# Performance work log

Measured on AMD Instinct MI355X. Metric: run time of the kernel, lower is better.

## Reference

```python
import jax, jax.numpy as jnp
import numpy as np

EPS = 1e-5  # PNA std-aggregator epsilon
N_NODES, N_EDGES, F_DIM, N_LAYERS = 50000, 800000, 64, 3


def setup_inputs() -> dict:
    key = jax.random.key(0)
    ks = jax.random.split(key, 6)
    x = jax.random.normal(ks[0], (N_NODES, F_DIM), jnp.float32)
    edge_index = jax.random.randint(ks[1], (2, N_EDGES), 0, N_NODES, jnp.int32)
    # Per-layer parameters, stacked on a leading layer axis.
    pre_w = jax.random.normal(ks[2], (N_LAYERS, 2 * F_DIM, F_DIM), jnp.float32) / np.sqrt(2 * F_DIM).astype(np.float32)
    pre_b = jnp.zeros((N_LAYERS, F_DIM), jnp.float32)
    post_w = jax.random.normal(ks[3], (N_LAYERS, 13 * F_DIM, F_DIM), jnp.float32) / np.sqrt(13 * F_DIM).astype(np.float32)
    post_b = jnp.zeros((N_LAYERS, F_DIM), jnp.float32)
    lin_w = jax.random.normal(ks[4], (N_LAYERS, F_DIM, F_DIM), jnp.float32) / np.sqrt(F_DIM).astype(np.float32)
    lin_b = jnpp = jnp.zeros((N_LAYERS, F_DIM), jnp.float32)
    return dict(x=x, edge_index=edge_index, pre_w=pre_w, pre_b=pre_b,
                post_w=post_w, post_b=post_b, lin_w=lin_w, lin_b=lin_b)


def reference(x, edge_index, pre_w, pre_b, post_w, post_b, lin_w, lin_b):
    src, dst = edge_index[0], edge_index[1]
    n = x.shape[0]
    # In-degree of aggregation targets (clamped to >=1, as in PyG DegreeScalerAggregation).
    deg = jax.ops.segment_sum(jnp.ones_like(dst, dtype=x.dtype), dst, num_segments=n)
    has_edge = (deg > 0)[:, None]
    deg_c = jnp.maximum(deg, 1.0)[:, None]              # [N,1]
    log_deg = jnp.log(deg_c + 1.0)                      # [N,1]
    avg_log = jnp.mean(log_deg)
    amp = log_deg / avg_log                              # amplification scaler
    att = avg_log / log_deg                              # attenuation scaler

    h = x
    for l in range(pre_w.shape[0]):
        # message: pre_nn(cat([x_i, x_j]))  -> [E, F]
        m = jnp.concatenate([h[dst], h[src]], axis=-1) @ pre_w[l] + pre_b[l]
        # fused multi-aggregator scatter-reduce per target node
        s1 = jax.ops.segment_sum(m, dst, num_segments=n)
        s2 = jax.ops.segment_sum(m * m, dst, num_segments=n)
        mean = s1 / deg_c
        std = jnp.sqrt(jax.nn.relu(s2 / deg_c - mean * mean) + EPS)
        mx = jnp.where(has_edge, jax.ops.segment_max(m, dst, num_segments=n), 0.0)
        mn = jnp.where(has_edge, jax.ops.segment_min(m, dst, num_segments=n), 0.0)
        agg = jnp.concatenate([mean, mx, mn, std], axis=-1)        # [N, 4F]
        scaled = jnp.concatenate([agg, agg * amp, agg * att], -1)  # [N, 12F]
        # post_nn(cat([x, scaled])) then final lin, plus residual shortcut
        out = jnp.concatenate([h, scaled], axis=-1) @ post_w[l] + post_b[l]
        out = out @ lin_w[l] + lin_b[l]
        h = out + h
    return h
```

## Files before the change

kernel.cpp:

```cpp
#include <hip/hip_runtime.h>
#include <math.h>

#define EPSV 1e-5f
#define EPB3 4096
#define NBP 256
#define CAP 6144
#define CAPS (CAP + 768)

typedef short s16x8 __attribute__((ext_vector_type(8)));
typedef float f32x4 __attribute__((ext_vector_type(4)));
typedef unsigned short u16;
typedef unsigned short u16x4 __attribute__((ext_vector_type(4)));

#define MFMA(a, b, c) __builtin_amdgcn_mfma_f32_16x16x32_bf16(a, b, c, 0, 0, 0)

__device__ inline u16 f2bf(float f) {
    unsigned u = __float_as_uint(f);
    return (u16)((u + 0x7FFF + ((u >> 16) & 1)) >> 16);
}
__device__ inline float bf2f(u16 h) { return __uint_as_float(((unsigned)h) << 16); }

__device__ inline void split8(const float4& a, const float4& b, s16x8& hv, s16x8& lv) {
    float f[8] = {a.x, a.y, a.z, a.w, b.x, b.y, b.z, b.w};
#pragma unroll
    for (int i = 0; i < 8; ++i) {
        u16 h = f2bf(f[i]);
        hv[i] = (short)h;
        lv[i] = (short)f2bf(f[i] - bf2f(h));
    }
}

__global__ __launch_bounds__(512) void k_pre1(
    const int* __restrict__ src, const int* __restrict__ dst, int E,
    int* __restrict__ bucketCursor, unsigned* __restrict__ edgeTmp,
    const float* __restrict__ pre_w, const float* __restrict__ post_w,
    const float* __restrict__ post_b, const float* __restrict__ lin_w,
    const float* __restrict__ lin_b, u16* __restrict__ WpT_hi,
    u16* __restrict__ WpT_lo, u16* __restrict__ WT_hi, u16* __restrict__ WT_lo,
    float* __restrict__ bpp, int NB1) {
    __shared__ int cnt[NBP], loff[NBP], lpos[NBP], gbase[NBP], sbuf[NBP];
    __shared__ unsigned stage[EPB3];
    int t = threadIdx.x;
    if ((int)blockIdx.x < NB1) {
        int base = blockIdx.x * EPB3;
        int cntE = min(EPB3, E - base);
        if (t < NBP) cnt[t] = 0;
        __syncthreads();
        unsigned ed[8];
#pragma unroll
        for (int j = 0; j < 8; ++j) {
            int idx = j * 512 + t;
            if (idx < cntE) {
                int e = base + idx;
                unsigned s = (unsigned)src[e];
                unsigned d = (unsigned)dst[e];
                ed[j] = ((d >> 8) << 24) | ((d & 255u) << 16) | s;
                atomicAdd(&cnt[d >> 8], 1);
            } else ed[j] = 0xFFFFFFFFu;
        }
        __syncthreads();
        if (t < NBP) sbuf[t] = cnt[t];
        __syncthreads();
        for (int o = 1; o < NBP; o <<= 1) {
            int v = 0;
            if (t < NBP && t >= o) v = sbuf[t - o];
            __syncthreads();
            if (t < NBP) sbuf[t] += v;
            __syncthreads();
        }
        if (t < NBP) {
            loff[t] = sbuf[t] - cnt[t];
            lpos[t] = sbuf[t] - cnt[t];
            gbase[t] = (cnt[t] > 0) ? atomicAdd(&bucketCursor[t], cnt[t]) : 0;
        }
        __syncthreads();
#pragma unroll
        for (int j = 0; j < 8; ++j) {
            if (ed[j] != 0xFFFFFFFFu) {
                int b = ed[j] >> 24;
                int p = atomicAdd(&lpos[b], 1);
                stage[p] = ed[j];
            }
        }
        __syncthreads();
        for (int i = t; i < cntE; i += 512) {
            unsigned pr = stage[i];
            int b = pr >> 24;
            int pos = gbase[b] + (i - loff[b]);
            if (pos < CAP) edgeTmp[(size_t)b * CAP + pos] = pr;
        }
        return;
    }
    int wq = blockIdx.x - NB1;
    int l = wq / 449;
    int bx = wq - l * 449;
    if (bx < 320) {
        if (t < 192) {
            int k = bx, j = t;
            int third = j >> 6, c = j & 63;
            float out = 0.f;
            int r = -1;
            if (k < 64) r = (third == 0) ? k : -1;
            else        r = 64 + third * 256 + (k - 64);
            if (r >= 0) {
                const float* pw = post_w + (size_t)(l * 832 + r) * 64;
                const float* lw = lin_w + (size_t)l * 64 * 64;
                float s = 0.f;
                for (int kk = 0; kk < 64; ++kk) s += pw[kk] * lw[kk * 64 + c];
                out = s;
            }
            u16 h = f2bf(out);
            size_t o = ((size_t)l * 192 + j) * 320 + k;
            WT_hi[o] = h;
            WT_lo[o] = f2bf(out - bf2f(h));
        }
    } else if (bx < 448) {
        if (t < 64) {
            int c = bx - 320, k = t;
            float v = pre_w[(size_t)l * 8192 + (size_t)(k + (c >= 64 ? 64 : 0)) * 64 + (c & 63)];
            u16 h = f2bf(v);
            size_t o = ((size_t)l * 128 + c) * 64 + k;
            WpT_hi[o] = h;
            WpT_lo[o] = f2bf(v - bf2f(h));
        }
    } else {
        if (t < 64) {
            int c = t;
            const float* pb = post_b + l * 64;
            const float* lw = lin_w + (size_t)l * 64 * 64;
            float s = lin_b[l * 64 + c];
            for (int k = 0; k < 64; ++k) s += pb[k] * lw[k * 64 + c];
            bpp[l * 64 + c] = s;
        }
    }
}

__global__ __launch_bounds__(512) void k_pre2(
    const unsigned* __restrict__ edgeTmp, const int* __restrict__ bucketCur,
    int* __restrict__ deg, int* __restrict__ offs, float* __restrict__ lsum,
    u16* __restrict__ srcSorted,
    const float* __restrict__ x, const u16* __restrict__ WpT_hi,
    const u16* __restrict__ WpT_lo, const float* __restrict__ pre_b,
    u16* __restrict__ Ph, u16* __restrict__ Qh,
    int N, int E, int NB) {
    __shared__ __align__(16) char smem[55296];
    int t = threadIdx.x;
    if ((int)blockIdx.x < NB) {
        int* scnt = (int*)smem;
        int* sbuf = (int*)(smem + 1024);
        int* lcur = (int*)(smem + 2048);
        int* lofs = (int*)(smem + 3072);
        float* fred = (float*)(smem + 4096);
        u16* stageSrc = (u16*)(smem + 5120);
        int* cntPs = (int*)(smem + 5120 + CAPS * 2);
        int b = blockIdx.x;
        int n0 = b << 8;
        int nodes = min(256, N - n0);
        if (t < NBP) { lcur[t] = 0; scnt[t] = 0; }
        __syncthreads();
        int cnt = min(bucketCur[b], CAP);
        const unsigned* ebase = edgeTmp + (size_t)b * CAP;
        for (int i = t; i < cnt; i += 512) atomicAdd(&lcur[(ebase[i] >> 16) & 255], 1);
        __syncthreads();
        float ls = 0.f;
        int d = 0, dP = 0;
        if (t < nodes) {
            d = lcur[t];
            deg[n0 + t] = d;
            ls = logf(fmaxf((float)d, 1.f) + 1.f);
            dP = (d + 3) & ~3;
        }
        if (t < 256) fred[t] = ls;
        if (t < NBP) sbuf[t] = dP;
        __syncthreads();
        for (int o = 1; o < NBP; o <<= 1) {
            int v = 0;
            if (t < NBP && t >= o) v = sbuf[t - o];
            __syncthreads();
            if (t < NBP) sbuf[t] += v;
            __syncthreads();
        }
        if (t < NBP) lofs[t] = sbuf[t] - dP;
        if (t < nodes) offs[n0 + t] = b * CAPS + (sbuf[t] - dP);
        if (t == NBP - 1) *cntPs = sbuf[t];
        __syncthreads();
        for (int o = 128; o > 0; o >>= 1) {
            if (t < o) fred[t] += fred[t + o];
            __syncthreads();
        }
        if (t == 0) atomicAdd(lsum, fred[0]);
        for (int i = t; i < cnt; i += 512) {
            unsigned p = ebase[i];
            int dl = (p >> 16) & 255;
            int r = atomicAdd(&scnt[dl], 1);
            stageSrc[lofs[dl] + r] = (u16)(p & 0xFFFFu);
        }
        __syncthreads();
        if (t < nodes && (d & 3)) {
            int lp = lofs[t];
            u16 lastv = stageSrc[lp + d - 1];
            for (int k = d; k < dP; ++k) stageSrc[lp + k] = lastv;
        }
        __syncthreads();
        int cntP = *cntPs;
        for (int i = t; i < cntP; i += 512) srcSorted[(size_t)b * CAPS + i] = stageSrc[i];
        return;
    }
    u16* Ah = (u16*)smem;
    u16* Al = (u16*)(smem + 9216);
    u16* Bh = (u16*)(smem + 18432);
    u16* Bl = (u16*)(smem + 36864);
    int rows0 = ((int)blockIdx.x - NB) * 64;
    int wid = t >> 6, lane = t & 63;
    int quad = lane >> 4, l16 = lane & 15;
    int wm = wid & 1, wn = wid >> 1;
    if (t < 256) {
#pragma unroll
        for (int it = 0; it < 2; ++it) {
            int task = it * 256 + t;
            int r = task >> 3, seg = task & 7;
            int row = rows0 + r;
            float4 v0 = make_float4(0.f, 0.f, 0.f, 0.f), v1 = v0;
            if (row < N) {
                v0 = *(const float4*)&x[(size_t)row * 64 + seg * 8];
                v1 = *(const float4*)&x[(size_t)row * 64 + seg * 8 + 4];
            }
            s16x8 hv, lv;
            split8(v0, v1, hv, lv);
            *(s16x8*)&Ah[r * 72 + seg * 8] = hv;
            *(s16x8*)&Al[r * 72 + seg * 8] = lv;
        }
#pragma unroll
        for (int it = 0; it < 4; ++it) {
            int task = it * 256 + t;
            int c = task >> 3, seg = task & 7;
            *(s16x8*)&Bh[c * 72 + seg * 8] = *(const s16x8*)&WpT_hi[(size_t)c * 64 + seg * 8];
            *(s16x8*)&Bl[c * 72 + seg * 8] = *(const s16x8*)&WpT_lo[(size_t)c * 64 + seg * 8];
        }
    }
    __syncthreads();
    if (t < 256) {
        f32x4 acc[2][4];
#pragma unroll
        for (int mt = 0; mt < 2; ++mt)
#pragma unroll
            for (int tt = 0; tt < 4; ++tt) acc[mt][tt] = (f32x4){0.f, 0.f, 0.f, 0.f};
#pragma unroll
        for (int c = 0; c < 2; ++c) {
            s16x8 ah[2], al[2];
#pragma unroll
            for (int mt = 0; mt < 2; ++mt) {
                int r = wm * 32 + mt * 16 + l16;
                ah[mt] = *(s16x8*)&Ah[r * 72 + c * 32 + quad * 8];
                al[mt] = *(s16x8*)&Al[r * 72 + c * 32 + quad * 8];
            }
#pragma unroll
            for (int tt = 0; tt < 4; ++tt) {
                int cc = wn * 64 + tt * 16 + l16;
                s16x8 bh = *(s16x8*)&Bh[cc * 72 + c * 32 + quad * 8];
                s16x8 bl = *(s16x8*)&Bl[cc * 72 + c * 32 + quad * 8];
#pragma unroll
                for (int mt = 0; mt < 2; ++mt) {
                    acc[mt][tt] = MFMA(ah[mt], bh, acc[mt][tt]);
                    acc[mt][tt] = MFMA(ah[mt], bl, acc[mt][tt]);
                    if (wn == 0) acc[mt][tt] = MFMA(al[mt], bh, acc[mt][tt]);
                }
            }
        }
#pragma unroll
        for (int mt = 0; mt < 2; ++mt)
#pragma unroll
            for (int tt = 0; tt < 4; ++tt) {
                int col = wn * 64 + tt * 16 + l16;
#pragma unroll
                for (int r = 0; r < 4; ++r) {
                    int row = rows0 + wm * 32 + mt * 16 + quad * 4 + r;
                    if (row >= N) continue;
                    float v = acc[mt][tt][r];
                    if (col < 64) Ph[(size_t)row * 64 + col] = f2bf(v + pre_b[col]);
                    else          Qh[(size_t)row * 64 + (col - 64)] = f2bf(v);
                }
            }
    }
}


__global__ __launch_bounds__(256) void k_agg(const u16* __restrict__ Ph,
                                             const u16* __restrict__ Qh,
                                             const int* __restrict__ offs,
                                             const int* __restrict__ degp,
                                             const u16* __restrict__ ss,
                                             u16* __restrict__ AGGh, int N) {
    int w = threadIdx.x >> 6, lane = threadIdx.x & 63;
    int g = lane >> 4;
    int f4b = (lane & 15) << 3;
    int node = blockIdx.x * 16 + w * 4 + g;
    int nc = min(node, N - 1);
    int beg = offs[nc];
    int d = (node < N) ? degp[nc] : 0;
    int dP = (d + 3) & ~3;
    int end = beg + dP;
    int mdP = dP;
    mdP = max(mdP, __shfl_xor(mdP, 16));
    mdP = max(mdP, __shfl_xor(mdP, 32));
    int trips = mdP >> 2;

    float sum0 = 0.f, sum1 = 0.f, sum2 = 0.f, sum3 = 0.f;
    float sq0 = 0.f, sq1 = 0.f, sq2 = 0.f, sq3 = 0.f;
    float mx0 = -3.4e38f, mx1 = -3.4e38f, mx2 = -3.4e38f, mx3 = -3.4e38f;
    float mn0 = 3.4e38f, mn1 = 3.4e38f, mn2 = 3.4e38f, mn3 = 3.4e38f;

    const char* qbase = (const char*)Qh;

#define ACC4(LO, HI)                                                        \
    {                                                                       \
        float q0 = __uint_as_float((LO) << 16);                             \
        float q1 = __uint_as_float((LO) & 0xFFFF0000u);                     \
        float q2 = __uint_as_float((HI) << 16);                             \
        float q3 = __uint_as_float((HI) & 0xFFFF0000u);                     \
        sum0 += q0; sq0 = fmaf(q0, q0, sq0);                                \
        mx0 = fmaxf(mx0, q0); mn0 = fminf(mn0, q0);                         \
        sum1 += q1; sq1 = fmaf(q1, q1, sq1);                                \
        mx1 = fmaxf(mx1, q1); mn1 = fminf(mn1, q1);                         \
        sum2 += q2; sq2 = fmaf(q2, q2, sq2);                                \
        mx2 = fmaxf(mx2, q2); mn2 = fminf(mn2, q2);                         \
        sum3 += q3; sq3 = fmaf(q3, q3, sq3);                                \
        mx3 = fmaxf(mx3, q3); mn3 = fminf(mn3, q3);                         \
    }

    int e = beg;
    for (int it = 0; it < trips; ++it, e += 4) {
        if (e < end) {
            uint2 sw = *(const uint2*)(ss + e);
            unsigned a0 = ((sw.x & 0xFFFFu) << 7) | (unsigned)f4b;
            unsigned a1 = ((sw.x >> 16) << 7) | (unsigned)f4b;
            unsigned a2 = ((sw.y & 0xFFFFu) << 7) | (unsigned)f4b;
            unsigned a3 = ((sw.y >> 16) << 7) | (unsigned)f4b;
            uint2 qa = *(const uint2*)(qbase + a0);
            uint2 qb = *(const uint2*)(qbase + a1);
            uint2 qc = *(const uint2*)(qbase + a2);
            uint2 qd = *(const uint2*)(qbase + a3);
            ACC4(qa.x, qa.y);
            ACC4(qb.x, qb.y);
            ACC4(qc.x, qc.y);
            ACC4(qd.x, qd.y);
        }
    }
#undef ACC4

    if (d & 3) {
        unsigned sl = ss[beg + d - 1];
        uint2 ql = *(const uint2*)(qbase + ((sl << 7) | (unsigned)f4b));
        float padf = (float)(dP - d);
        float qL0 = __uint_as_float(ql.x << 16);
        float qL1 = __uint_as_float(ql.x & 0xFFFF0000u);
        float qL2 = __uint_as_float(ql.y << 16);
        float qL3 = __uint_as_float(ql.y & 0xFFFF0000u);
        float t0 = padf * qL0, t1 = padf * qL1, t2 = padf * qL2, t3 = padf * qL3;
        sum0 -= t0; sq0 = fmaf(-t0, qL0, sq0);
        sum1 -= t1; sq1 = fmaf(-t1, qL1, sq1);
        sum2 -= t2; sq2 = fmaf(-t2, qL2, sq2);
        sum3 -= t3; sq3 = fmaf(-t3, qL3, sq3);
    }

    float dc = fmaxf((float)d, 1.f);
    float inv = 1.0f / dc;
    float e0 = sum0 * inv, e1 = sum1 * inv, e2 = sum2 * inv, e3 = sum3 * inv;
    float sd0 = sqrtf(fmaxf(fmaf(-e0, e0, sq0 * inv), 0.f) + EPSV);
    float sd1 = sqrtf(fmaxf(fmaf(-e1, e1, sq1 * inv), 0.f) + EPSV);
    float sd2 = sqrtf(fmaxf(fmaf(-e2, e2, sq2 * inv), 0.f) + EPSV);
    float sd3 = sqrtf(fmaxf(fmaf(-e3, e3, sq3 * inv), 0.f) + EPSV);

    uint2 pw = *(const uint2*)((const char*)Ph + (((unsigned)nc << 7) | (unsigned)f4b));
    float p0 = __uint_as_float(pw.x << 16), p1 = __uint_as_float(pw.x & 0xFFFF0000u);
    float p2 = __uint_as_float(pw.y << 16), p3 = __uint_as_float(pw.y & 0xFFFF0000u);

    bool he = d > 0;
    float m0 = he ? p0 + e0 : 0.f, m1 = he ? p1 + e1 : 0.f;
    float m2 = he ? p2 + e2 : 0.f, m3 = he ? p3 + e3 : 0.f;
    float X0 = he ? p0 + mx0 : 0.f, X1 = he ? p1 + mx1 : 0.f;
    float X2 = he ? p2 + mx2 : 0.f, X3 = he ? p3 + mx3 : 0.f;
    float n0 = he ? p0 + mn0 : 0.f, n1 = he ? p1 + mn1 : 0.f;
    float n2 = he ? p2 + mn2 : 0.f, n3 = he ? p3 + mn3 : 0.f;

    if (node < N) {
        u16* out = (u16*)((char*)AGGh + (((unsigned)node << 9) | (unsigned)f4b));
        *(u16x4*)(out)       = (u16x4){f2bf(m0), f2bf(m1), f2bf(m2), f2bf(m3)};
        *(u16x4*)(out + 64)  = (u16x4){f2bf(X0), f2bf(X1), f2bf(X2), f2bf(X3)};
        *(u16x4*)(out + 128) = (u16x4){f2bf(n0), f2bf(n1), f2bf(n2), f2bf(n3)};
        *(u16x4*)(out + 192) = (u16x4){f2bf(sd0), f2bf(sd1), f2bf(sd2), f2bf(sd3)};
    }
}

__global__ __launch_bounds__(512) void k_gemm2(const float* __restrict__ hIn,
                                               const u16* __restrict__ AGGh,
                                               const u16* __restrict__ WT_hi,
                                               const u16* __restrict__ WT_lo,
                                               const float* __restrict__ bpp,
                                               const int* __restrict__ degp,
                                               const float* __restrict__ lsum,
                                               float* __restrict__ hOut,
                                               int doNext,
                                               const u16* __restrict__ WpN_hi,
                                               const u16* __restrict__ WpN_lo,
                                               const float* __restrict__ pre_bN,
                                               u16* __restrict__ PhN,
                                               u16* __restrict__ QhN, int M) {
    __shared__ u16 Ah[128 * 40], Al[128 * 40];
    __shared__ u16 Bh[192 * 40], Bl[192 * 40];
    int t = threadIdx.x, wid = t >> 6, lane = t & 63;
    int rows0 = blockIdx.x * 128;
    int quad = lane >> 4, l16 = lane & 15;
    int wm = wid & 3, wn = wid >> 2;

    f32x4 acc[2][6];
#pragma unroll
    for (int mt = 0; mt < 2; ++mt)
#pragma unroll
        for (int tt = 0; tt < 6; ++tt) acc[mt][tt] = (f32x4){0.f, 0.f, 0.f, 0.f};

#pragma unroll
    for (int chunk = 0; chunk < 2; ++chunk) {
        {
            int r = t >> 2, seg = t & 3;
            int row = rows0 + r;
            float4 v0 = make_float4(0.f, 0.f, 0.f, 0.f), v1 = v0;
            if (row < M) {
                v0 = *(const float4*)&hIn[(size_t)row * 64 + chunk * 32 + seg * 8];
                v1 = *(const float4*)&hIn[(size_t)row * 64 + chunk * 32 + seg * 8 + 4];
            }
            s16x8 hv, lv;
            split8(v0, v1, hv, lv);
            *(s16x8*)&Ah[r * 40 + seg * 8] = hv;
            *(s16x8*)&Al[r * 40 + seg * 8] = lv;
        }
        if (t < 256) {
            int c = t >> 2, seg = t & 3;
            int k0g = chunk * 32;
            *(s16x8*)&Bh[c * 40 + seg * 8] = *(const s16x8*)&WT_hi[(size_t)c * 320 + k0g + seg * 8];
            *(s16x8*)&Bl[c * 40 + seg * 8] = *(const s16x8*)&WT_lo[(size_t)c * 320 + k0g + seg * 8];
        }
        __syncthreads();

        s16x8 ah[2], al[2];
#pragma unroll
        for (int mt = 0; mt < 2; ++mt) {
            int r = wm * 32 + mt * 16 + l16;
            ah[mt] = *(s16x8*)&Ah[r * 40 + quad * 8];
            al[mt] = *(s16x8*)&Al[r * 40 + quad * 8];
        }
#pragma unroll
        for (int cg = 0; cg < 2; ++cg) {
            int cc = wn * 32 + cg * 16 + l16;
            s16x8 bh = *(s16x8*)&Bh[cc * 40 + quad * 8];
            s16x8 bl = *(s16x8*)&Bl[cc * 40 + quad * 8];
#pragma unroll
            for (int mt = 0; mt < 2; ++mt) {
                acc[mt][cg] = MFMA(ah[mt], bh, acc[mt][cg]);
                acc[mt][cg] = MFMA(al[mt], bh, acc[mt][cg]);
                acc[mt][cg] = MFMA(ah[mt], bl, acc[mt][cg]);
            }
        }
        __syncthreads();
    }

    for (int chunk = 0; chunk < 8; ++chunk) {
        {
            int r = t >> 2, seg = t & 3;
            int row = rows0 + r;
            s16x8 v = (s16x8){0, 0, 0, 0, 0, 0, 0, 0};
            if (row < M) v = *(const s16x8*)&AGGh[(size_t)row * 256 + chunk * 32 + seg * 8];
            *(s16x8*)&Ah[r * 40 + seg * 8] = v;
        }
        {
            int k0g = 64 + chunk * 32;
#pragma unroll
            for (int it = 0; it < 2; ++it) {
                int task = it * 512 + t;
                if (task < 768) {
                    int c = task >> 2, seg = task & 3;
                    *(s16x8*)&Bh[c * 40 + seg * 8] = *(const s16x8*)&WT_hi[(size_t)c * 320 + k0g + seg * 8];
                    *(s16x8*)&Bl[c * 40 + seg * 8] = *(const s16x8*)&WT_lo[(size_t)c * 320 + k0g + seg * 8];
                }
            }
        }
        __syncthreads();

        s16x8 ah[2];
#pragma unroll
        for (int mt = 0; mt < 2; ++mt) {
            int r = wm * 32 + mt * 16 + l16;
            ah[mt] = *(s16x8*)&Ah[r * 40 + quad * 8];
        }
#pragma unroll
        for (int tt = 0; tt < 6; ++tt) {
            int cc = wn * 32 + (tt & 1) * 16 + (tt >> 1) * 64 + l16;
            s16x8 bh = *(s16x8*)&Bh[cc * 40 + quad * 8];
            s16x8 bl = *(s16x8*)&Bl[cc * 40 + quad * 8];
#pragma unroll
            for (int mt = 0; mt < 2; ++mt) {
                acc[mt][tt] = MFMA(ah[mt], bh, acc[mt][tt]);
                acc[mt][tt] = MFMA(ah[mt], bl, acc[mt][tt]);
            }
        }
        __syncthreads();
    }

    float hv[2][2][4];
    float avg = *lsum / (float)M;
#pragma unroll
    for (int mt = 0; mt < 2; ++mt)
#pragma unroll
        for (int r = 0; r < 4; ++r) {
            int row = rows0 + wm * 32 + mt * 16 + quad * 4 + r;
            float am = 1.f, at = 1.f, hin0 = 0.f, hin1 = 0.f;
            if (row < M) {
                float dc = fmaxf((float)degp[row], 1.f);
                float ld = logf(dc + 1.f);
                am = ld / avg;
                at = avg / ld;
                hin0 = hIn[(size_t)row * 64 + wn * 32 + l16];
                hin1 = hIn[(size_t)row * 64 + wn * 32 + 16 + l16];
            }
#pragma unroll
            for (int cg = 0; cg < 2; ++cg) {
                int col = wn * 32 + cg * 16 + l16;
                float v = acc[mt][cg][r] + am * acc[mt][cg + 2][r] + at * acc[mt][cg + 4][r]
                        + (cg == 0 ? hin0 : hin1) + bpp[col];
                hv[mt][cg][r] = v;
                if (row < M) hOut[(size_t)row * 64 + col] = v;
            }
        }

    if (doNext) {
        f32x4 acc2[2][4];
#pragma unroll
        for (int mt = 0; mt < 2; ++mt)
#pragma unroll
            for (int tt = 0; tt < 4; ++tt) acc2[mt][tt] = (f32x4){0.f, 0.f, 0.f, 0.f};

#pragma unroll
        for (int chunk = 0; chunk < 2; ++chunk) {
            {
                int c = t >> 2, seg = t & 3;
                *(s16x8*)&Bh[c * 40 + seg * 8] = *(const s16x8*)&WpN_hi[(size_t)c * 64 + chunk * 32 + seg * 8];
                *(s16x8*)&Bl[c * 40 + seg * 8] = *(const s16x8*)&WpN_lo[(size_t)c * 64 + chunk * 32 + seg * 8];
            }
            if (wn == chunk) {
#pragma unroll
                for (int mt = 0; mt < 2; ++mt)
#pragma unroll
                    for (int cg = 0; cg < 2; ++cg) {
                        int lc = cg * 16 + l16;
#pragma unroll
                        for (int r = 0; r < 4; ++r) {
                            int rl = wm * 32 + mt * 16 + quad * 4 + r;
                            float v = hv[mt][cg][r];
                            u16 hi = f2bf(v);
                            Ah[rl * 40 + lc] = hi;
                            Al[rl * 40 + lc] = f2bf(v - bf2f(hi));
                        }
                    }
            }
            __syncthreads();

            s16x8 ah[2], al[2];
#pragma unroll
            for (int mt = 0; mt < 2; ++mt) {
                int r = wm * 32 + mt * 16 + l16;
                ah[mt] = *(s16x8*)&Ah[r * 40 + quad * 8];
                al[mt] = *(s16x8*)&Al[r * 40 + quad * 8];
            }
#pragma unroll
            for (int tt = 0; tt < 4; ++tt) {
                int cc = wn * 64 + tt * 16 + l16;
                s16x8 bh = *(s16x8*)&Bh[cc * 40 + quad * 8];
                s16x8 bl = *(s16x8*)&Bl[cc * 40 + quad * 8];
#pragma unroll
                for (int mt = 0; mt < 2; ++mt) {
                    acc2[mt][tt] = MFMA(ah[mt], bh, acc2[mt][tt]);
                    acc2[mt][tt] = MFMA(ah[mt], bl, acc2[mt][tt]);
                    if (wn == 0) acc2[mt][tt] = MFMA(al[mt], bh, acc2[mt][tt]);
                }
            }
            __syncthreads();
        }

#pragma unroll
        for (int mt = 0; mt < 2; ++mt)
#pragma unroll
            for (int tt = 0; tt < 4; ++tt) {
                int col = wn * 64 + tt * 16 + l16;
#pragma unroll
                for (int r = 0; r < 4; ++r) {
                    int row = rows0 + wm * 32 + mt * 16 + quad * 4 + r;
                    if (row >= M) continue;
                    float v = acc2[mt][tt][r];
                    if (col < 64) PhN[(size_t)row * 64 + col] = f2bf(v + pre_bN[col]);
                    else          QhN[(size_t)row * 64 + (col - 64)] = f2bf(v);
                }
            }
    }
}


extern "C" void kernel_launch(void* const* d_in, const int* in_sizes, int n_in,
                              void* d_out, int out_size, void* d_ws, size_t ws_size,
                              hipStream_t stream) {
    const float* x      = (const float*)d_in[0];
    const int*   ei     = (const int*)d_in[1];
    const float* pre_w  = (const float*)d_in[2];
    const float* pre_b  = (const float*)d_in[3];
    const float* post_w = (const float*)d_in[4];
    const float* post_b = (const float*)d_in[5];
    const float* lin_w  = (const float*)d_in[6];
    const float* lin_b  = (const float*)d_in[7];

    const int N = in_sizes[0] / 64;
    const int E = in_sizes[1] / 2;
    const int L = in_sizes[2] / (128 * 64);

    const int* srcIdx = ei;
    const int* dstIdx = ei + E;

    char* ws = (char*)d_ws;
    size_t off = 0;
    auto alloc = [&](size_t bytes) {
        void* p = ws + off;
        off += (bytes + 255) & ~(size_t)255;
        return p;
    };
    int*      deg        = (int*)alloc((size_t)N * 4);
    int*      offs       = (int*)alloc((size_t)(N + 1) * 4);
    u16*      srcSorted  = (u16*)alloc((size_t)NBP * CAPS * 2);
    unsigned* edgeTmp    = (unsigned*)alloc((size_t)NBP * CAP * 4);
    int*      bucketCur  = (int*)alloc(NBP * 4);
    float*    lsum       = (float*)alloc(256);
    u16*      WpT_hi     = (u16*)alloc((size_t)L * 128 * 64 * 2);
    u16*      WpT_lo     = (u16*)alloc((size_t)L * 128 * 64 * 2);
    u16*      WT_hi      = (u16*)alloc((size_t)L * 192 * 320 * 2);
    u16*      WT_lo      = (u16*)alloc((size_t)L * 192 * 320 * 2);
    float*    bpp        = (float*)alloc((size_t)L * 64 * 4);
    u16*      Ph         = (u16*)alloc((size_t)N * 64 * 2);
    u16*      Qh         = (u16*)alloc((size_t)N * 64 * 2);
    u16*      AGGh       = (u16*)alloc((size_t)N * 256 * 2);
    float*    hA         = (float*)alloc((size_t)N * 64 * 4);
    float*    hB         = (float*)alloc((size_t)N * 64 * 4);
    (void)ws_size;

    int NB = (N + 255) >> 8;
    int NB1 = (E + EPB3 - 1) / EPB3;
    int gblk = (N + 63) / 64;
    int gblk2 = (N + 127) / 128;

    hipMemsetAsync(bucketCur, 0, NBP * 4, stream);
    hipMemsetAsync(lsum, 0, 4, stream);

    k_pre1<<<NB1 + 449 * L, 512, 0, stream>>>(
        srcIdx, dstIdx, E, bucketCur, edgeTmp,
        pre_w, post_w, post_b, lin_w, lin_b,
        WpT_hi, WpT_lo, WT_hi, WT_lo, bpp, NB1);

    k_pre2<<<NB + gblk, 512, 0, stream>>>(
        edgeTmp, bucketCur, deg, offs, lsum, srcSorted,
        x, WpT_hi, WpT_lo, pre_b, Ph, Qh, N, E, NB);

    const float* hIn = x;
    float* hbuf[2] = {hA, hB};
    for (int l = 0; l < L; ++l) {
        float* hOut = (l == L - 1) ? (float*)d_out : hbuf[l & 1];
        int dn = (l < L - 1) ? 1 : 0;
        int ln = dn ? (l + 1) : 0;
        k_agg<<<(N + 15) / 16, 256, 0, stream>>>(Ph, Qh, offs, deg, srcSorted, AGGh, N);
        k_gemm2<<<gblk2, 512, 0, stream>>>(hIn, AGGh,
                                           WT_hi + (size_t)l * 192 * 320,
                                           WT_lo + (size_t)l * 192 * 320,
                                           bpp + (size_t)l * 64,
                                           deg, lsum, hOut, dn,
                                           WpT_hi + (size_t)ln * 128 * 64,
                                           WpT_lo + (size_t)ln * 128 * 64,
                                           pre_b + (size_t)ln * 64,
                                           Ph, Qh, N);
        hIn = hOut;
    }
}
```

Baseline: 268.3 us.

## Load GEMM2 operands directly from global into registers, dropping LDS staging and barriers

The post-aggregation GEMM kernel previously staged activation rows and weight tiles through shared memory with a __syncthreads pair per K-chunk. Each wave now loads its MFMA A and B fragments straight from global memory (rows clamped to M-1), which removes the LDS round trip and all barriers in both K loops. The trade-off is that weight fragments are now re-read from global/L2 by every wave instead of once per block, which adds cache traffic and may expose load latency. The B shared buffers are shrunk, although they appear to remain only for the epilogue.

```diff
diff --git a/kernel.cpp b/kernel.cpp
--- a/kernel.cpp
+++ b/kernel.cpp
@@ -407,7 +407,7 @@
                                                u16* __restrict__ PhN,
                                                u16* __restrict__ QhN, int M) {
     __shared__ u16 Ah[128 * 40], Al[128 * 40];
-    __shared__ u16 Bh[192 * 40], Bl[192 * 40];
+    __shared__ u16 Bh[128 * 40], Bl[128 * 40];
     int t = threadIdx.x, wid = t >> 6, lane = t & 63;
     int rows0 = blockIdx.x * 128;
     int quad = lane >> 4, l16 = lane & 15;
@@ -419,41 +419,27 @@
 #pragma unroll
         for (int tt = 0; tt < 6; ++tt) acc[mt][tt] = (f32x4){0.f, 0.f, 0.f, 0.f};
 
+    int rA[2];
+#pragma unroll
+    for (int mt = 0; mt < 2; ++mt)
+        rA[mt] = min(rows0 + wm * 32 + mt * 16 + l16, M - 1);
+
 #pragma unroll
     for (int chunk = 0; chunk < 2; ++chunk) {
-        {
-            int r = t >> 2, seg = t & 3;
-            int row = rows0 + r;
-            float4 v0 = make_float4(0.f, 0.f, 0.f, 0.f), v1 = v0;
-            if (row < M) {
-                v0 = *(const float4*)&hIn[(size_t)row * 64 + chunk * 32 + seg * 8];
-                v1 = *(const float4*)&hIn[(size_t)row * 64 + chunk * 32 + seg * 8 + 4];
-            }
-            s16x8 hv, lv;
-            split8(v0, v1, hv, lv);
-            *(s16x8*)&Ah[r * 40 + seg * 8] = hv;
-            *(s16x8*)&Al[r * 40 + seg * 8] = lv;
-        }
-        if (t < 256) {
-            int c = t >> 2, seg = t & 3;
-            int k0g = chunk * 32;
-            *(s16x8*)&Bh[c * 40 + seg * 8] = *(const s16x8*)&WT_hi[(size_t)c * 320 + k0g + seg * 8];
-            *(s16x8*)&Bl[c * 40 + seg * 8] = *(const s16x8*)&WT_lo[(size_t)c * 320 + k0g + seg * 8];
-        }
-        __syncthreads();
-
         s16x8 ah[2], al[2];
 #pragma unroll
         for (int mt = 0; mt < 2; ++mt) {
-            int r = wm * 32 + mt * 16 + l16;
-            ah[mt] = *(s16x8*)&Ah[r * 40 + quad * 8];
-            al[mt] = *(s16x8*)&Al[r * 40 + quad * 8];
+            const float* hp = &hIn[(size_t)rA[mt] * 64 + chunk * 32 + quad * 8];
+            float4 v0 = *(const float4*)hp;
+            float4 v1 = *(const float4*)(hp + 4);
+            split8(v0, v1, ah[mt], al[mt]);
         }
 #pragma unroll
         for (int cg = 0; cg < 2; ++cg) {
             int cc = wn * 32 + cg * 16 + l16;
-            s16x8 bh = *(s16x8*)&Bh[cc * 40 + quad * 8];
-            s16x8 bl = *(s16x8*)&Bl[cc * 40 + quad * 8];
+            size_t bo = (size_t)cc * 320 + chunk * 32 + quad * 8;
+            s16x8 bh = *(const s16x8*)&WT_hi[bo];
+            s16x8 bl = *(const s16x8*)&WT_lo[bo];
 #pragma unroll
             for (int mt = 0; mt < 2; ++mt) {
                 acc[mt][cg] = MFMA(ah[mt], bh, acc[mt][cg]);
@@ -461,49 +447,27 @@
                 acc[mt][cg] = MFMA(ah[mt], bl, acc[mt][cg]);
             }
         }
-        __syncthreads();
-    }
-
+    }
+
+#pragma unroll 2
     for (int chunk = 0; chunk < 8; ++chunk) {
-        {
-            int r = t >> 2, seg = t & 3;
-            int row = rows0 + r;
-            s16x8 v = (s16x8){0, 0, 0, 0, 0, 0, 0, 0};
-            if (row < M) v = *(const s16x8*)&AGGh[(size_t)row * 256 + chunk * 32 + seg * 8];
-            *(s16x8*)&Ah[r * 40 + seg * 8] = v;
-        }
-        {
-            int k0g = 64 + chunk * 32;
-#pragma unroll
-            for (int it = 0; it < 2; ++it) {
-                int task = it * 512 + t;
-                if (task < 768) {
-                    int c = task >> 2, seg = task & 3;
-                    *(s16x8*)&Bh[c * 40 + seg * 8] = *(const s16x8*)&WT_hi[(size_t)c * 320 + k0g + seg * 8];
-                    *(s16x8*)&Bl[c * 40 + seg * 8] = *(const s16x8*)&WT_lo[(size_t)c * 320 + k0g + seg * 8];
-                }
-            }
-        }
-        __syncthreads();
-
+        int k0 = chunk * 32;
         s16x8 ah[2];
 #pragma unroll
-        for (int mt = 0; mt < 2; ++mt) {
-            int r = wm * 32 + mt * 16 + l16;
-            ah[mt] = *(s16x8*)&Ah[r * 40 + quad * 8];
-        }
+        for (int mt = 0; mt < 2; ++mt)
+            ah[mt] = *(const s16x8*)&AGGh[(size_t)rA[mt] * 256 + k0 + quad * 8];
 #pragma unroll
         for (int tt = 0; tt < 6; ++tt) {
             int cc = wn * 32 + (tt & 1) * 16 + (tt >> 1) * 64 + l16;
-            s16x8 bh = *(s16x8*)&Bh[cc * 40 + quad * 8];
-            s16x8 bl = *(s16x8*)&Bl[cc * 40 + quad * 8];
+            size_t bo = (size_t)cc * 320 + 64 + k0 + quad * 8;
+            s16x8 bh = *(const s16x8*)&WT_hi[bo];
+            s16x8 bl = *(const s16x8*)&WT_lo[bo];
 #pragma unroll
             for (int mt = 0; mt < 2; ++mt) {
                 acc[mt][tt] = MFMA(ah[mt], bh, acc[mt][tt]);
                 acc[mt][tt] = MFMA(ah[mt], bl, acc[mt][tt]);
             }
         }
-        __syncthreads();
     }
 
     float hv[2][2][4];
```

After: 384.1 us. 1.43x slower.

## Remap post-GEMM warps to 2x4 layout and register-prefetch next K chunk

Applied to the files above, without the earlier changes.

Changes the warp tiling of the fused post_nn/lin GEMM from 4x2 to 2x4, so each warp covers 64 rows and one 16-column slice across the three scaler blocks. This lets B fragments be reused across four M tiles and simplifies the epilogue. The 8-chunk aggregation loop now prefetches the next chunk's AGG and weight slices into registers while the current chunk computes, overlapping global loads with MFMA work. The cost is higher register pressure from the larger accumulator set and the prefetch registers, which could lower occupancy.

```diff
diff --git a/kernel.cpp b/kernel.cpp
--- a/kernel.cpp
+++ b/kernel.cpp
@@ -411,28 +411,31 @@
     int t = threadIdx.x, wid = t >> 6, lane = t & 63;
     int rows0 = blockIdx.x * 128;
     int quad = lane >> 4, l16 = lane & 15;
-    int wm = wid & 3, wn = wid >> 2;
-
-    f32x4 acc[2][6];
-#pragma unroll
-    for (int mt = 0; mt < 2; ++mt)
-#pragma unroll
-        for (int tt = 0; tt < 6; ++tt) acc[mt][tt] = (f32x4){0.f, 0.f, 0.f, 0.f};
+    int wm = wid & 1;
+    int wn = wid >> 1;
+
+    f32x4 acc[4][3];
+#pragma unroll
+    for (int mt = 0; mt < 4; ++mt)
+#pragma unroll
+        for (int th = 0; th < 3; ++th) acc[mt][th] = (f32x4){0.f, 0.f, 0.f, 0.f};
+
+    int sr = t >> 2, sseg = t & 3;
+    int bc1 = 128 + (t >> 2);
 
 #pragma unroll
     for (int chunk = 0; chunk < 2; ++chunk) {
         {
-            int r = t >> 2, seg = t & 3;
-            int row = rows0 + r;
+            int row = rows0 + sr;
             float4 v0 = make_float4(0.f, 0.f, 0.f, 0.f), v1 = v0;
             if (row < M) {
-                v0 = *(const float4*)&hIn[(size_t)row * 64 + chunk * 32 + seg * 8];
-                v1 = *(const float4*)&hIn[(size_t)row * 64 + chunk * 32 + seg * 8 + 4];
+                v0 = *(const float4*)&hIn[(size_t)row * 64 + chunk * 32 + sseg * 8];
+                v1 = *(const float4*)&hIn[(size_t)row * 64 + chunk * 32 + sseg * 8 + 4];
             }
             s16x8 hv, lv;
             split8(v0, v1, hv, lv);
-            *(s16x8*)&Ah[r * 40 + seg * 8] = hv;
-            *(s16x8*)&Al[r * 40 + seg * 8] = lv;
+            *(s16x8*)&Ah[sr * 40 + sseg * 8] = hv;
+            *(s16x8*)&Al[sr * 40 + sseg * 8] = lv;
         }
         if (t < 256) {
             int c = t >> 2, seg = t & 3;
@@ -442,162 +445,168 @@
         }
         __syncthreads();
 
-        s16x8 ah[2], al[2];
-#pragma unroll
-        for (int mt = 0; mt < 2; ++mt) {
-            int r = wm * 32 + mt * 16 + l16;
+        s16x8 ah[4], al[4];
+#pragma unroll
+        for (int mt = 0; mt < 4; ++mt) {
+            int r = wm * 64 + mt * 16 + l16;
             ah[mt] = *(s16x8*)&Ah[r * 40 + quad * 8];
             al[mt] = *(s16x8*)&Al[r * 40 + quad * 8];
         }
-#pragma unroll
-        for (int cg = 0; cg < 2; ++cg) {
-            int cc = wn * 32 + cg * 16 + l16;
+        {
+            int cc = wn * 16 + l16;
             s16x8 bh = *(s16x8*)&Bh[cc * 40 + quad * 8];
             s16x8 bl = *(s16x8*)&Bl[cc * 40 + quad * 8];
 #pragma unroll
-            for (int mt = 0; mt < 2; ++mt) {
-                acc[mt][cg] = MFMA(ah[mt], bh, acc[mt][cg]);
-                acc[mt][cg] = MFMA(al[mt], bh, acc[mt][cg]);
-                acc[mt][cg] = MFMA(ah[mt], bl, acc[mt][cg]);
-            }
-        }
-        __syncthreads();
-    }
-
-    for (int chunk = 0; chunk < 8; ++chunk) {
+            for (int mt = 0; mt < 4; ++mt) {
+                acc[mt][0] = MFMA(ah[mt], bh, acc[mt][0]);
+                acc[mt][0] = MFMA(al[mt], bh, acc[mt][0]);
+                acc[mt][0] = MFMA(ah[mt], bl, acc[mt][0]);
+            }
+        }
+        __syncthreads();
+    }
+
+    {
+        s16x8 pa, pbh0, pbl0, pbh1, pbl1;
+        int rowA = rows0 + sr;
         {
-            int r = t >> 2, seg = t & 3;
-            int row = rows0 + r;
-            s16x8 v = (s16x8){0, 0, 0, 0, 0, 0, 0, 0};
-            if (row < M) v = *(const s16x8*)&AGGh[(size_t)row * 256 + chunk * 32 + seg * 8];
-            *(s16x8*)&Ah[r * 40 + seg * 8] = v;
-        }
-        {
-            int k0g = 64 + chunk * 32;
-#pragma unroll
-            for (int it = 0; it < 2; ++it) {
-                int task = it * 512 + t;
-                if (task < 768) {
-                    int c = task >> 2, seg = task & 3;
-                    *(s16x8*)&Bh[c * 40 + seg * 8] = *(const s16x8*)&WT_hi[(size_t)c * 320 + k0g + seg * 8];
-                    *(s16x8*)&Bl[c * 40 + seg * 8] = *(const s16x8*)&WT_lo[(size_t)c * 320 + k0g + seg * 8];
+            pa = (s16x8){0, 0, 0, 0, 0, 0, 0, 0};
+            if (rowA < M) pa = *(const s16x8*)&AGGh[(size_t)rowA * 256 + sseg * 8];
+            size_t bo0 = (size_t)sr * 320 + 64 + sseg * 8;
+            pbh0 = *(const s16x8*)&WT_hi[bo0];
+            pbl0 = *(const s16x8*)&WT_lo[bo0];
+            if (t < 256) {
+                size_t bo1 = (size_t)bc1 * 320 + 64 + sseg * 8;
+                pbh1 = *(const s16x8*)&WT_hi[bo1];
+                pbl1 = *(const s16x8*)&WT_lo[bo1];
+            }
+        }
+        for (int chunk = 0; chunk < 8; ++chunk) {
+            __syncthreads();
+            *(s16x8*)&Ah[sr * 40 + sseg * 8] = pa;
+            *(s16x8*)&Bh[sr * 40 + sseg * 8] = pbh0;
+            *(s16x8*)&Bl[sr * 40 + sseg * 8] = pbl0;
+            if (t < 256) {
+                *(s16x8*)&Bh[bc1 * 40 + sseg * 8] = pbh1;
+                *(s16x8*)&Bl[bc1 * 40 + sseg * 8] = pbl1;
+            }
+            __syncthreads();
+            if (chunk < 7) {
+                int k0n = 64 + (chunk + 1) * 32;
+                pa = (s16x8){0, 0, 0, 0, 0, 0, 0, 0};
+                if (rowA < M) pa = *(const s16x8*)&AGGh[(size_t)rowA * 256 + (chunk + 1) * 32 + sseg * 8];
+                size_t bo0 = (size_t)sr * 320 + k0n + sseg * 8;
+                pbh0 = *(const s16x8*)&WT_hi[bo0];
+                pbl0 = *(const s16x8*)&WT_lo[bo0];
+                if (t < 256) {
+                    size_t bo1 = (size_t)bc1 * 320 + k0n + sseg * 8;
+                    pbh1 = *(const s16x8*)&WT_hi[bo1];
+                    pbl1 = *(const s16x8*)&WT_lo[bo1];
                 }
             }
-        }
-        __syncthreads();
-
-        s16x8 ah[2];
-#pragma unroll
-        for (int mt = 0; mt < 2; ++mt) {
-            int r = wm * 32 + mt * 16 + l16;
-            ah[mt] = *(s16x8*)&Ah[r * 40 + quad * 8];
-        }
-#pragma unroll
-        for (int tt = 0; tt < 6; ++tt) {
-            int cc = wn * 32 + (tt & 1) * 16 + (tt >> 1) * 64 + l16;
-            s16x8 bh = *(s16x8*)&Bh[cc * 40 + quad * 8];
-            s16x8 bl = *(s16x8*)&Bl[cc * 40 + quad * 8];
-#pragma unroll
-            for (int mt = 0; mt < 2; ++mt) {
-                acc[mt][tt] = MFMA(ah[mt], bh, acc[mt][tt]);
-                acc[mt][tt] = MFMA(ah[mt], bl, acc[mt][tt]);
-            }
-        }
-        __syncthreads();
-    }
-
-    float hv[2][2][4];
+            s16x8 ah[4];
+#pragma unroll
+            for (int mt = 0; mt < 4; ++mt)
+                ah[mt] = *(s16x8*)&Ah[(wm * 64 + mt * 16 + l16) * 40 + quad * 8];
+#pragma unroll
+            for (int th = 0; th < 3; ++th) {
+                int cc = wn * 16 + th * 64 + l16;
+                s16x8 bh = *(s16x8*)&Bh[cc * 40 + quad * 8];
+                s16x8 bl = *(s16x8*)&Bl[cc * 40 + quad * 8];
+#pragma unroll
+                for (int mt = 0; mt < 4; ++mt) {
+                    acc[mt][th] = MFMA(ah[mt], bh, acc[mt][th]);
+                    acc[mt][th] = MFMA(ah[mt], bl, acc[mt][th]);
+                }
+            }
+        }
+    }
+    __syncthreads();
+
+    float hv[4][4];
+    int col = wn * 16 + l16;
     float avg = *lsum / (float)M;
-#pragma unroll
-    for (int mt = 0; mt < 2; ++mt)
+    float bp = bpp[col];
+#pragma unroll
+    for (int mt = 0; mt < 4; ++mt)
 #pragma unroll
         for (int r = 0; r < 4; ++r) {
-            int row = rows0 + wm * 32 + mt * 16 + quad * 4 + r;
-            float am = 1.f, at = 1.f, hin0 = 0.f, hin1 = 0.f;
+            int row = rows0 + wm * 64 + mt * 16 + quad * 4 + r;
+            float am = 1.f, at = 1.f, hin = 0.f;
             if (row < M) {
                 float dc = fmaxf((float)degp[row], 1.f);
                 float ld = logf(dc + 1.f);
                 am = ld / avg;
                 at = avg / ld;
-                hin0 = hIn[(size_t)row * 64 + wn * 32 + l16];
-                hin1 = hIn[(size_t)row * 64 + wn * 32 + 16 + l16];
-            }
-#pragma unroll
-            for (int cg = 0; cg < 2; ++cg) {
-                int col = wn * 32 + cg * 16 + l16;
-                float v = acc[mt][cg][r] + am * acc[mt][cg + 2][r] + at * acc[mt][cg + 4][r]
-                        + (cg == 0 ? hin0 : hin1) + bpp[col];
-                hv[mt][cg][r] = v;
-                if (row < M) hOut[(size_t)row * 64 + col] = v;
-            }
+                hin = hIn[(size_t)row * 64 + col];
+            }
+            float v = acc[mt][0][r] + am * acc[mt][1][r] + at * acc[mt][2][r] + hin + bp;
+            hv[mt][r] = v;
+            if (row < M) hOut[(size_t)row * 64 + col] = v;
         }
 
     if (doNext) {
-        f32x4 acc2[2][4];
-#pragma unroll
-        for (int mt = 0; mt < 2; ++mt)
-#pragma unroll
-            for (int tt = 0; tt < 4; ++tt) acc2[mt][tt] = (f32x4){0.f, 0.f, 0.f, 0.f};
+        f32x4 acc2[4][2];
+#pragma unroll
+        for (int mt = 0; mt < 4; ++mt)
+#pragma unroll
+            for (int tt = 0; tt < 2; ++tt) acc2[mt][tt] = (f32x4){0.f, 0.f, 0.f, 0.f};
 
 #pragma unroll
         for (int chunk = 0; chunk < 2; ++chunk) {
             {
-                int c = t >> 2, seg = t & 3;
-                *(s16x8*)&Bh[c * 40 + seg * 8] = *(const s16x8*)&WpN_hi[(size_t)c * 64 + chunk * 32 + seg * 8];
-                *(s16x8*)&Bl[c * 40 + seg * 8] = *(const s16x8*)&WpN_lo[(size_t)c * 64 + chunk * 32 + seg * 8];
-            }
-            if (wn == chunk) {
-#pragma unroll
-                for (int mt = 0; mt < 2; ++mt)
-#pragma unroll
-                    for (int cg = 0; cg < 2; ++cg) {
-                        int lc = cg * 16 + l16;
-#pragma unroll
-                        for (int r = 0; r < 4; ++r) {
-                            int rl = wm * 32 + mt * 16 + quad * 4 + r;
-                            float v = hv[mt][cg][r];
-                            u16 hi = f2bf(v);
-                            Ah[rl * 40 + lc] = hi;
-                            Al[rl * 40 + lc] = f2bf(v - bf2f(hi));
-                        }
+                *(s16x8*)&Bh[sr * 40 + sseg * 8] = *(const s16x8*)&WpN_hi[(size_t)sr * 64 + chunk * 32 + sseg * 8];
+                *(s16x8*)&Bl[sr * 40 + sseg * 8] = *(const s16x8*)&WpN_lo[(size_t)sr * 64 + chunk * 32 + sseg * 8];
+            }
+            if ((wn >> 1) == chunk) {
+                int lc = (wn & 1) * 16 + l16;
+#pragma unroll
+                for (int mt = 0; mt < 4; ++mt)
+#pragma unroll
+                    for (int r = 0; r < 4; ++r) {
+                        int rl = wm * 64 + mt * 16 + quad * 4 + r;
+                        float v = hv[mt][r];
+                        u16 hi = f2bf(v);
+                        Ah[rl * 40 + lc] = hi;
+                        Al[rl * 40 + lc] = f2bf(v - bf2f(hi));
                     }
             }
             __syncthreads();
 
-            s16x8 ah[2], al[2];
-#pragma unroll
-            for (int mt = 0; mt < 2; ++mt) {
-                int r = wm * 32 + mt * 16 + l16;
+            s16x8 ah[4], al[4];
+#pragma unroll
+            for (int mt = 0; mt < 4; ++mt) {
+                int r = wm * 64 + mt * 16 + l16;
                 ah[mt] = *(s16x8*)&Ah[r * 40 + quad * 8];
                 al[mt] = *(s16x8*)&Al[r * 40 + quad * 8];
             }
 #pragma unroll
-            for (int tt = 0; tt < 4; ++tt) {
-                int cc = wn * 64 + tt * 16 + l16;
+            for (int tt = 0; tt < 2; ++tt) {
+                int cc = wn * 32 + tt * 16 + l16;
                 s16x8 bh = *(s16x8*)&Bh[cc * 40 + quad * 8];
                 s16x8 bl = *(s16x8*)&Bl[cc * 40 + quad * 8];
 #pragma unroll
-                for (int mt = 0; mt < 2; ++mt) {
+                for (int mt = 0; mt < 4; ++mt) {
                     acc2[mt][tt] = MFMA(ah[mt], bh, acc2[mt][tt]);
                     acc2[mt][tt] = MFMA(ah[mt], bl, acc2[mt][tt]);
-                    if (wn == 0) acc2[mt][tt] = MFMA(al[mt], bh, acc2[mt][tt]);
+                    if (wn < 2) acc2[mt][tt] = MFMA(al[mt], bh, acc2[mt][tt]);
                 }
             }
             __syncthreads();
         }
 
 #pragma unroll
-        for (int mt = 0; mt < 2; ++mt)
-#pragma unroll
-            for (int tt = 0; tt < 4; ++tt) {
-                int col = wn * 64 + tt * 16 + l16;
+        for (int mt = 0; mt < 4; ++mt)
+#pragma unroll
+            for (int tt = 0; tt < 2; ++tt) {
+                int colc = wn * 32 + tt * 16 + l16;
 #pragma unroll
                 for (int r = 0; r < 4; ++r) {
-                    int row = rows0 + wm * 32 + mt * 16 + quad * 4 + r;
+                    int row = rows0 + wm * 64 + mt * 16 + quad * 4 + r;
                     if (row >= M) continue;
                     float v = acc2[mt][tt][r];
-                    if (col < 64) PhN[(size_t)row * 64 + col] = f2bf(v + pre_bN[col]);
-                    else          QhN[(size_t)row * 64 + (col - 64)] = f2bf(v);
+                    if (colc < 64) PhN[(size_t)row * 64 + colc] = f2bf(v + pre_bN[colc]);
+                    else           QhN[(size_t)row * 64 + (colc - 64)] = f2bf(v);
                 }
             }
     }
```

Result: slower. 293.1 us (+9.3%).
